# Optimization experiments

Hardware: AMD Instinct MI355X
Metric: run time of the kernel (lower is better)

## Reference

```python
import jax, jax.numpy as jnp
import numpy as np

T, B, I, H, O = 512, 64, 512, 1024, 512


def setup_inputs() -> dict:
    key = jax.random.key(0)
    ks = jax.random.split(key, 12)
    k = 1.0 / np.sqrt(H)  # torch LSTM/Linear init scale
    u = lambda kk, shape: jax.random.uniform(kk, shape, jnp.float32, -k, k)
    return {
        "x": jax.random.normal(ks[0], (T, B, I), jnp.float32),
        # layer 0 (input -> hidden)
        "W_ih0": u(ks[1], (4 * H, I)),
        "W_hh0": u(ks[2], (4 * H, H)),
        "b_ih0": u(ks[3], (4 * H,)),
        "b_hh0": u(ks[4], (4 * H,)),
        # layer 1 (hidden -> hidden)
        "W_ih1": u(ks[5], (4 * H, H)),
        "W_hh1": u(ks[6], (4 * H, H)),
        "b_ih1": u(ks[7], (4 * H,)),
        "b_hh1": u(ks[8], (4 * H,)),
        # output projection
        "W_out": u(ks[9], (O, H)),
        "b_out": u(ks[10], (O,)),
    }


def _lstm_layer(x_seq, W_ih, W_hh, b_ih, b_hh):
    """x_seq: [T, B, in]; returns hidden sequence [T, B, H].
    PyTorch gate order: i, f, g, o."""
    Hh = W_hh.shape[1]
    Bb = x_seq.shape[1]
    # precompute input contribution for all timesteps (one big GEMM)
    pre = jnp.einsum('tbi,gi->tbg', x_seq, W_ih) + b_ih + b_hh  # [T, B, 4H]

    def step(carry, pre_t):
        h, c = carry
        gates = pre_t + h @ W_hh.T  # [B, 4H]
        i, f, g, o = jnp.split(gates, 4, axis=-1)
        i = jax.nn.sigmoid(i)
        f = jax.nn.sigmoid(f)
        g = jnp.tanh(g)
        o = jax.nn.sigmoid(o)
        c = f * c + i * g
        h = o * jnp.tanh(c)
        return (h, c), h

    h0 = jnp.zeros((Bb, Hh), x_seq.dtype)
    c0 = jnp.zeros((Bb, Hh), x_seq.dtype)
    _, hs = jax.lax.scan(step, (h0, c0), pre)
    return hs  # [T, B, H]


def reference(x, W_ih0, W_hh0, b_ih0, b_hh0, W_ih1, W_hh1, b_ih1, b_hh1, W_out, b_out):
    h1 = _lstm_layer(x, W_ih0, W_hh0, b_ih0, b_hh0)   # [T, B, H]
    h2 = _lstm_layer(h1, W_ih1, W_hh1, b_ih1, b_hh1)  # [T, B, H]
    return jnp.einsum('tbh,oh->tbo', h2, W_out) + b_out  # [T, B, O]
```

## Files before the change

kernel.cpp:

```cpp
#include <hip/hip_runtime.h>
#include <hip/hip_bf16.h>
#include <cstdint>
#include <cstddef>

typedef short bf16x8 __attribute__((ext_vector_type(8)));
typedef float f32x4  __attribute__((ext_vector_type(4)));
typedef __hip_bfloat16 bf16;

#define NT_T 512
#define NB   64
#define NI   512
#define NH   1024
#define NO   512

static constexpr size_t SLOT_E = (size_t)NB * NH + 128;
static constexpr size_t SLOT_B = SLOT_E * 2;

static constexpr size_t OFF_XBF   = 0;
static constexpr size_t SZ_XBF    = (size_t)NT_T * NB * NI * 2;
static constexpr size_t OFF_WSW0  = OFF_XBF + SZ_XBF;
static constexpr size_t SZ_WSW0   = 128ull * 98304;
static constexpr size_t OFF_WSW1  = OFF_WSW0 + SZ_WSW0;
static constexpr size_t SZ_WSW1   = 128ull * 131072;
static constexpr size_t OFF_WOUT  = OFF_WSW1 + SZ_WSW1;
static constexpr size_t SZ_WOUT   = (size_t)NO * NH * 2;
static constexpr size_t OFF_B0    = OFF_WOUT + SZ_WOUT;
static constexpr size_t OFF_B1    = OFF_B0 + 4096 * 4;
static constexpr size_t OFF_H1    = OFF_B1 + 4096 * 4;
static constexpr size_t SZ_H1     = (size_t)NT_T * SLOT_B;
static constexpr size_t OFF_H2    = OFF_H1 + SZ_H1;
static constexpr size_t SZ_H2     = (size_t)NT_T * SLOT_B;
static constexpr size_t OFF_FLG   = OFF_H2 + SZ_H2;
static constexpr size_t SZ_FLG    = 2ull * 128 * 512 * 2;

__device__ __forceinline__ float sigm(float x) {
  return 1.0f / (1.0f + __expf(-x));
}
__device__ __forceinline__ float tanh_fast(float x) {
  x = fminf(15.0f, fmaxf(-15.0f, x));
  const float e = __expf(2.0f * x);
  return (e - 1.0f) / (e + 1.0f);
}

__device__ __forceinline__ void waitf1(const unsigned short* f) {
  while (!__all(__hip_atomic_load(f, __ATOMIC_RELAXED, __HIP_MEMORY_SCOPE_AGENT) != 0))
    __builtin_amdgcn_s_sleep(1);
  asm volatile("" ::: "memory");
}
__device__ __forceinline__ void waitf2(const unsigned short* f0, const unsigned short* f1) {
  while (true) {
    const int a = __hip_atomic_load(f0, __ATOMIC_RELAXED, __HIP_MEMORY_SCOPE_AGENT);
    const int b = __hip_atomic_load(f1, __ATOMIC_RELAXED, __HIP_MEMORY_SCOPE_AGENT);
    if (__all((a != 0) && (b != 0))) break;
    __builtin_amdgcn_s_sleep(1);
  }
  asm volatile("" ::: "memory");
}

template <int N>
__device__ __forceinline__ void load_batch(bf16x8 (&A)[N][2], const bf16* p0, const bf16* p1) {
#pragma unroll
  for (int i = 0; i < N; ++i) {
    A[i][0] = *(const bf16x8*)(p0 + i * 32);
    A[i][1] = *(const bf16x8*)(p1 + i * 32);
  }
}

template <int N, int KSW>
__device__ __forceinline__ void mfma_batch(f32x4 (&acc)[2][2], const bf16x8 (&A)[N][2],
                                           const char* Wlds, int ksbase, int lane) {
#pragma unroll
  for (int i = 0; i < N; ++i) {
#pragma unroll
    for (int nt = 0; nt < 2; ++nt) {
      const bf16x8 b = *(const bf16x8*)(Wlds + ((size_t)(nt * KSW + ksbase + i) * 64 + lane) * 16);
      acc[0][nt] = __builtin_amdgcn_mfma_f32_16x16x32_bf16(A[i][0], b, acc[0][nt], 0, 0, 0);
      acc[1][nt] = __builtin_amdgcn_mfma_f32_16x16x32_bf16(A[i][1], b, acc[1][nt], 0, 0, 0);
    }
  }
}

__global__ void k_convert_x(const float* __restrict__ x, bf16* __restrict__ xbf) {
  const size_t n = (size_t)NT_T * NB * NI;
  for (size_t i = (size_t)blockIdx.x * blockDim.x + threadIdx.x; i < n;
       i += (size_t)gridDim.x * blockDim.x)
    xbf[i] = __float2bfloat16(x[i]);
}

__global__ void k_build_wsw(const float* __restrict__ Wih0, const float* __restrict__ Whh0,
                            const float* __restrict__ Wih1, const float* __restrict__ Whh1,
                            bf16* __restrict__ wsw0, bf16* __restrict__ wsw1) {
  const size_t L0N = 128ull * 2 * 48 * 64 * 8;
  const size_t L1N = 128ull * 2 * 64 * 64 * 8;
  const size_t n = L0N + L1N;
  for (size_t i = (size_t)blockIdx.x * blockDim.x + threadIdx.x; i < n;
       i += (size_t)gridDim.x * blockDim.x) {
    if (i < L0N) {
      size_t idx = i;
      const int j = idx & 7;    idx >>= 3;
      const int lane = idx & 63; idx >>= 6;
      const int ks = (int)(idx % 48); idx /= 48;
      const int nt = idx & 1;
      const int blk = (int)(idx >> 1);
      const int nl = nt * 16 + (lane & 15);
      const int k = ks * 32 + (lane >> 4) * 8 + j;
      const int grow = (nl >> 3) * 1024 + blk * 8 + (nl & 7);
      const float v = (k < 512) ? Wih0[(size_t)grow * 512 + k]
                                : Whh0[(size_t)grow * 1024 + (k - 512)];
      wsw0[i] = __float2bfloat16(v);
    } else {
      size_t idx = i - L0N;
      const size_t o = idx;
      const int j = idx & 7;    idx >>= 3;
      const int lane = idx & 63; idx >>= 6;
      const int ks = (int)(idx % 64); idx /= 64;
      const int nt = idx & 1;
      const int blk = (int)(idx >> 1);
      const int nl = nt * 16 + (lane & 15);
      const int k = ks * 32 + (lane >> 4) * 8 + j;
      const int grow = (nl >> 3) * 1024 + blk * 8 + (nl & 7);
      const float v = (k < 1024) ? Wih1[(size_t)grow * 1024 + k]
                                 : Whh1[(size_t)grow * 1024 + (k - 1024)];
      wsw1[o] = __float2bfloat16(v);
    }
  }
}

__global__ void k_small(const float* __restrict__ Wout,
                        const float* __restrict__ bih0, const float* __restrict__ bhh0,
                        const float* __restrict__ bih1, const float* __restrict__ bhh1,
                        bf16* __restrict__ woutbf, float* __restrict__ bias0,
                        float* __restrict__ bias1, unsigned int* __restrict__ flg) {
  const int i = blockIdx.x * 256 + threadIdx.x;
  if (i < NO * NH) woutbf[i] = __float2bfloat16(Wout[i]);
  if (i < 4096) {
    bias0[i] = bih0[i] + bhh0[i];
    bias1[i] = bih1[i] + bhh1[i];
  }
  if (i < (int)(SZ_FLG / 4)) flg[i] = 0u;
}

__global__ __launch_bounds__(256, 1) void lstm_recur(
    const bf16* __restrict__ xbf, const bf16* __restrict__ wsw0, const bf16* __restrict__ wsw1,
    const float* __restrict__ bias0, const float* __restrict__ bias1,
    bf16* __restrict__ h1hist, bf16* __restrict__ h2hist, unsigned short* __restrict__ flg) {
  __shared__ char Wlds[131072];
  __shared__ float red[64][33];

  const int tid = threadIdx.x;
  const int bid = blockIdx.x;
  const int layer = bid >> 7;
  const int blk = bid & 127;
  const int lane = tid & 63;
  const int wid = tid >> 6;
  const int mh = wid & 1;
  const int kh = wid >> 1;
  const int q = lane >> 4;
  const int ml = lane & 15;
  const int colbase = blk * 8;
  const int row0 = mh * 32 + ml;
  const int row1 = mh * 32 + 16 + ml;

  {
    const char* src = layer ? (const char*)wsw1 + (size_t)blk * 131072
                            : (const char*)wsw0 + (size_t)blk * 98304;
    const int nb = layer ? 131072 : 98304;
    for (int off = tid * 16; off < nb; off += 256 * 16)
      *(uint4*)(Wlds + off) = *(const uint4*)(src + off);
  }

  float biasv[2];
  {
    const float* bs = layer ? bias1 : bias0;
#pragma unroll
    for (int nt = 0; nt < 2; ++nt) {
      const int nl = nt * 16 + ml;
      biasv[nt] = bs[(nl >> 3) * 1024 + colbase + (nl & 7)];
    }
  }
  __syncthreads();

  float cstate[2] = {0.f, 0.f};
  const f32x4 zacc = {0.f, 0.f, 0.f, 0.f};
  const char* WldsC = Wlds;

  const unsigned short* f_l0 = flg;
  const unsigned short* f_l1 = flg + ((size_t)128 << 9);
  unsigned short* fme = flg + (((size_t)layer * 128 + blk) << 9);

  for (int t = 0; t < NT_T; ++t) {
    const bf16* h1prev = h1hist + (size_t)(t - 1) * SLOT_E;
    const bf16* h1cur  = h1hist + (size_t)t * SLOT_E;
    const bf16* h2prev = h2hist + (size_t)(t - 1) * SLOT_E;

    f32x4 acc[2][2];
#pragma unroll
    for (int a1 = 0; a1 < 2; ++a1)
#pragma unroll
      for (int a2 = 0; a2 < 2; ++a2) acc[a1][a2] = zacc;

    if (layer == 0) {
      const bf16* xb = xbf + (size_t)t * NB * NI;
      const int kx = kh * 256 + q * 8;
      bf16x8 Ax[8][2];
      load_batch<8>(Ax, xb + (size_t)row0 * NI + kx, xb + (size_t)row1 * NI + kx);
      if (t > 0) {
        waitf1(f_l0 + (((size_t)(kh * 64 + lane)) << 9) + (t - 1));
        const int khh = kh * 512 + q * 8;
        bf16x8 Ah[16][2];
        load_batch<16>(Ah, h1prev + (size_t)row0 * NH + khh,
                       h1prev + (size_t)row1 * NH + khh);
        __builtin_amdgcn_sched_barrier(0);
        mfma_batch<8, 48>(acc, Ax, WldsC, kh * 8, lane);
        mfma_batch<16, 48>(acc, Ah, WldsC, 16 + kh * 16, lane);
      } else {
        __builtin_amdgcn_sched_barrier(0);
        mfma_batch<8, 48>(acc, Ax, WldsC, kh * 8, lane);
      }
    } else {
      if (kh == 0) {
        waitf2(f_l0 + ((size_t)lane << 9) + t,
               f_l0 + (((size_t)(64 + lane)) << 9) + t);
        bf16x8 Ah[32][2];
        load_batch<32>(Ah, h1cur + (size_t)row0 * NH + q * 8,
                       h1cur + (size_t)row1 * NH + q * 8);
        __builtin_amdgcn_sched_barrier(0);
        mfma_batch<32, 64>(acc, Ah, WldsC, 0, lane);
      } else if (t > 0) {
        waitf2(f_l1 + ((size_t)lane << 9) + (t - 1),
               f_l1 + (((size_t)(64 + lane)) << 9) + (t - 1));
        bf16x8 Ah[32][2];
        load_batch<32>(Ah, h2prev + (size_t)row0 * NH + q * 8,
                       h2prev + (size_t)row1 * NH + q * 8);
        __builtin_amdgcn_sched_barrier(0);
        mfma_batch<32, 64>(acc, Ah, WldsC, 32, lane);
      }
    }

    if (kh == 1) {
#pragma unroll
      for (int mt = 0; mt < 2; ++mt)
#pragma unroll
        for (int nt = 0; nt < 2; ++nt)
#pragma unroll
          for (int r = 0; r < 4; ++r)
            red[mh * 32 + mt * 16 + q * 4 + r][nt * 16 + ml] = acc[mt][nt][r];
    }
    __syncthreads();
    if (kh == 0) {
#pragma unroll
      for (int mt = 0; mt < 2; ++mt)
#pragma unroll
        for (int nt = 0; nt < 2; ++nt)
#pragma unroll
          for (int r = 0; r < 4; ++r) {
            const int mloc = mh * 32 + mt * 16 + q * 4 + r;
            const int nloc = nt * 16 + ml;
            red[mloc][nloc] = acc[mt][nt][r] + red[mloc][nloc] + biasv[nt];
          }
    }
    __syncthreads();

    {
      const int b = tid >> 2;
      const int cc0 = (tid & 3) * 2;
      unsigned short hb[2];
#pragma unroll
      for (int e2 = 0; e2 < 2; ++e2) {
        const int cc = cc0 + e2;
        const float gi = red[b][cc];
        const float gf = red[b][8 + cc];
        const float gg = red[b][16 + cc];
        const float go = red[b][24 + cc];
        const float cn = sigm(gf) * cstate[e2] + sigm(gi) * tanh_fast(gg);
        cstate[e2] = cn;
        const float hv = sigm(go) * tanh_fast(cn);
        hb[e2] = __builtin_bit_cast(unsigned short, __float2bfloat16(hv));
      }
      const unsigned int packed = (unsigned int)hb[0] | ((unsigned int)hb[1] << 16);
      bf16* dstbase = (layer ? h2hist : h1hist) + (size_t)t * SLOT_E + (size_t)b * NH;
      __hip_atomic_store((unsigned int*)(dstbase + colbase + cc0), packed,
                         __ATOMIC_RELAXED, __HIP_MEMORY_SCOPE_AGENT);
    }

    __syncthreads();
    if (tid == 0)
      __hip_atomic_store(fme + t, (unsigned short)1,
                         __ATOMIC_RELAXED, __HIP_MEMORY_SCOPE_AGENT);
  }
}

__global__ __launch_bounds__(256) void gemm_out(
    const bf16* __restrict__ A, const bf16* __restrict__ B,
    const float* __restrict__ bout, float* __restrict__ out) {
  __shared__ char As[8192];
  __shared__ char Bs[8192];
  const int tid = threadIdx.x;
  const int lane = tid & 63;
  const int wid = tid >> 6;
  const int wm = wid >> 1;
  const int wn = wid & 1;
  const size_t Mbase = (size_t)blockIdx.y * 128;
  const int Nbase = blockIdx.x * 128;

  const f32x4 zacc = {0.f, 0.f, 0.f, 0.f};
  f32x4 acc[4][4];
#pragma unroll
  for (int i = 0; i < 4; ++i)
#pragma unroll
    for (int j = 0; j < 4; ++j) acc[i][j] = zacc;

  for (int kc = 0; kc < 32; ++kc) {
    const int kb = kc * 32;
#pragma unroll
    for (int e = 0; e < 2; ++e) {
      const int id = e * 256 + tid;
      const int r = id >> 2;
      const int c8 = (id & 3) * 8;
      const int dst = ((r >> 4) * 64 + (c8 >> 3) * 16 + (r & 15)) * 16;
      const size_t m = Mbase + r;
      const bf16* arow = A + (m >> 6) * SLOT_E + (size_t)(m & 63) * NH;
      *(uint4*)(As + dst) = *(const uint4*)(arow + kb + c8);
      *(uint4*)(Bs + dst) = *(const uint4*)(B + (size_t)(Nbase + r) * NH + kb + c8);
    }
    __syncthreads();
    bf16x8 af[4], bfr[4];
#pragma unroll
    for (int i = 0; i < 4; ++i) {
      af[i]  = *(const bf16x8*)(As + ((wm * 4 + i) * 64 + lane) * 16);
      bfr[i] = *(const bf16x8*)(Bs + ((wn * 4 + i) * 64 + lane) * 16);
    }
#pragma unroll
    for (int i = 0; i < 4; ++i)
#pragma unroll
      for (int j = 0; j < 4; ++j)
        acc[i][j] = __builtin_amdgcn_mfma_f32_16x16x32_bf16(af[i], bfr[j], acc[i][j], 0, 0, 0);
    __syncthreads();
  }
  const int qq = lane >> 4, ml = lane & 15;
#pragma unroll
  for (int i = 0; i < 4; ++i)
#pragma unroll
    for (int j = 0; j < 4; ++j)
#pragma unroll
      for (int r = 0; r < 4; ++r) {
        const size_t m = Mbase + wm * 64 + i * 16 + qq * 4 + r;
        const int n = Nbase + wn * 64 + j * 16 + ml;
        out[m * NO + n] = acc[i][j][r] + bout[n];
      }
}

extern "C" void kernel_launch(void* const* d_in, const int* in_sizes, int n_in,
                              void* d_out, int out_size, void* d_ws, size_t ws_size,
                              hipStream_t stream) {
  (void)in_sizes; (void)n_in; (void)out_size; (void)ws_size;
  const float* x    = (const float*)d_in[0];
  const float* Wih0 = (const float*)d_in[1];
  const float* Whh0 = (const float*)d_in[2];
  const float* bih0 = (const float*)d_in[3];
  const float* bhh0 = (const float*)d_in[4];
  const float* Wih1 = (const float*)d_in[5];
  const float* Whh1 = (const float*)d_in[6];
  const float* bih1 = (const float*)d_in[7];
  const float* bhh1 = (const float*)d_in[8];
  const float* Wout = (const float*)d_in[9];
  const float* bout = (const float*)d_in[10];
  float* out = (float*)d_out;
  char* ws = (char*)d_ws;

  bf16*  xbf    = (bf16*)(ws + OFF_XBF);
  bf16*  wsw0   = (bf16*)(ws + OFF_WSW0);
  bf16*  wsw1   = (bf16*)(ws + OFF_WSW1);
  bf16*  woutbf = (bf16*)(ws + OFF_WOUT);
  float* bias0  = (float*)(ws + OFF_B0);
  float* bias1  = (float*)(ws + OFF_B1);
  bf16*  h1hist = (bf16*)(ws + OFF_H1);
  bf16*  h2hist = (bf16*)(ws + OFF_H2);
  unsigned short* flg = (unsigned short*)(ws + OFF_FLG);

  k_convert_x<<<8192, 256, 0, stream>>>(x, xbf);
  k_build_wsw<<<14336, 256, 0, stream>>>(Wih0, Whh0, Wih1, Whh1, wsw0, wsw1);
  k_small<<<2048, 256, 0, stream>>>(Wout, bih0, bhh0, bih1, bhh1, woutbf, bias0, bias1,
                                    (unsigned int*)flg);
  lstm_recur<<<256, 256, 0, stream>>>(xbf, wsw0, wsw1, bias0, bias1, h1hist, h2hist, flg);
  gemm_out<<<dim3(4, 256), 256, 0, stream>>>(h2hist, woutbf, bout, out);
}
```

Before: 5.488 ms.

## Replace per-step flag handshake with sentinel-filled hidden state polling

Removes the separate flag array and the per-block flag store after each timestep. The hidden-state history buffers are pre-filled with an all-ones sentinel, and consumers poll the actual h data with atomic loads until no 32-bit word equals the sentinel. This folds the dependency wait and the data load into one step, cutting a round trip through flag memory on the serial recurrence path. The cost is a fill kernel over both history buffers and heavier polling traffic. It relies on a packed bf16 pair never being 0xFFFFFFFF, which would be a NaN pair.

```diff
diff --git a/kernel.cpp b/kernel.cpp
--- a/kernel.cpp
+++ b/kernel.cpp
@@ -5,6 +5,7 @@
 
 typedef short bf16x8 __attribute__((ext_vector_type(8)));
 typedef float f32x4  __attribute__((ext_vector_type(4)));
+typedef unsigned int u32x4 __attribute__((ext_vector_type(4)));
 typedef __hip_bfloat16 bf16;
 
 #define NT_T 512
@@ -30,8 +31,6 @@
 static constexpr size_t SZ_H1     = (size_t)NT_T * SLOT_B;
 static constexpr size_t OFF_H2    = OFF_H1 + SZ_H1;
 static constexpr size_t SZ_H2     = (size_t)NT_T * SLOT_B;
-static constexpr size_t OFF_FLG   = OFF_H2 + SZ_H2;
-static constexpr size_t SZ_FLG    = 2ull * 128 * 512 * 2;
 
 __device__ __forceinline__ float sigm(float x) {
   return 1.0f / (1.0f + __expf(-x));
@@ -42,18 +41,37 @@
   return (e - 1.0f) / (e + 1.0f);
 }
 
-__device__ __forceinline__ void waitf1(const unsigned short* f) {
-  while (!__all(__hip_atomic_load(f, __ATOMIC_RELAXED, __HIP_MEMORY_SCOPE_AGENT) != 0))
+template <int N>
+__device__ __forceinline__ void poll_tile(bf16x8 (&A)[N][2], const bf16* p0, const bf16* p1) {
+  const unsigned int* q0 = (const unsigned int*)p0;
+  const unsigned int* q1 = (const unsigned int*)p1;
+  unsigned int V[N][2][4];
+  while (true) {
+#pragma unroll
+    for (int i = 0; i < N; ++i)
+#pragma unroll
+      for (int j = 0; j < 4; ++j) {
+        V[i][0][j] = __hip_atomic_load(q0 + i * 16 + j, __ATOMIC_RELAXED, __HIP_MEMORY_SCOPE_AGENT);
+        V[i][1][j] = __hip_atomic_load(q1 + i * 16 + j, __ATOMIC_RELAXED, __HIP_MEMORY_SCOPE_AGENT);
+      }
+    bool ok = true;
+#pragma unroll
+    for (int i = 0; i < N; ++i)
+#pragma unroll
+      for (int r = 0; r < 2; ++r)
+#pragma unroll
+        for (int j = 0; j < 4; ++j)
+          ok &= (V[i][r][j] != 0xFFFFFFFFu);
+    if (__all(ok)) break;
     __builtin_amdgcn_s_sleep(1);
-  asm volatile("" ::: "memory");
-}
-__device__ __forceinline__ void waitf2(const unsigned short* f0, const unsigned short* f1) {
-  while (true) {
-    const int a = __hip_atomic_load(f0, __ATOMIC_RELAXED, __HIP_MEMORY_SCOPE_AGENT);
-    const int b = __hip_atomic_load(f1, __ATOMIC_RELAXED, __HIP_MEMORY_SCOPE_AGENT);
-    if (__all((a != 0) && (b != 0))) break;
-    __builtin_amdgcn_s_sleep(1);
-  }
+  }
+#pragma unroll
+  for (int i = 0; i < N; ++i)
+#pragma unroll
+    for (int r = 0; r < 2; ++r) {
+      const u32x4 tv = {V[i][r][0], V[i][r][1], V[i][r][2], V[i][r][3]};
+      A[i][r] = __builtin_bit_cast(bf16x8, tv);
+    }
   asm volatile("" ::: "memory");
 }
 
@@ -85,6 +103,13 @@
   for (size_t i = (size_t)blockIdx.x * blockDim.x + threadIdx.x; i < n;
        i += (size_t)gridDim.x * blockDim.x)
     xbf[i] = __float2bfloat16(x[i]);
+}
+
+__global__ void k_fill(u32x4* __restrict__ p, size_t n16) {
+  const u32x4 s = {0xFFFFFFFFu, 0xFFFFFFFFu, 0xFFFFFFFFu, 0xFFFFFFFFu};
+  for (size_t i = (size_t)blockIdx.x * blockDim.x + threadIdx.x; i < n16;
+       i += (size_t)gridDim.x * blockDim.x)
+    p[i] = s;
 }
 
 __global__ void k_build_wsw(const float* __restrict__ Wih0, const float* __restrict__ Whh0,
@@ -130,20 +155,19 @@
                         const float* __restrict__ bih0, const float* __restrict__ bhh0,
                         const float* __restrict__ bih1, const float* __restrict__ bhh1,
                         bf16* __restrict__ woutbf, float* __restrict__ bias0,
-                        float* __restrict__ bias1, unsigned int* __restrict__ flg) {
+                        float* __restrict__ bias1) {
   const int i = blockIdx.x * 256 + threadIdx.x;
   if (i < NO * NH) woutbf[i] = __float2bfloat16(Wout[i]);
   if (i < 4096) {
     bias0[i] = bih0[i] + bhh0[i];
     bias1[i] = bih1[i] + bhh1[i];
   }
-  if (i < (int)(SZ_FLG / 4)) flg[i] = 0u;
 }
 
 __global__ __launch_bounds__(256, 1) void lstm_recur(
     const bf16* __restrict__ xbf, const bf16* __restrict__ wsw0, const bf16* __restrict__ wsw1,
     const float* __restrict__ bias0, const float* __restrict__ bias1,
-    bf16* __restrict__ h1hist, bf16* __restrict__ h2hist, unsigned short* __restrict__ flg) {
+    bf16* __restrict__ h1hist, bf16* __restrict__ h2hist) {
   __shared__ char Wlds[131072];
   __shared__ float red[64][33];
 
@@ -184,10 +208,6 @@
   const f32x4 zacc = {0.f, 0.f, 0.f, 0.f};
   const char* WldsC = Wlds;
 
-  const unsigned short* f_l0 = flg;
-  const unsigned short* f_l1 = flg + ((size_t)128 << 9);
-  unsigned short* fme = flg + (((size_t)layer * 128 + blk) << 9);
-
   for (int t = 0; t < NT_T; ++t) {
     const bf16* h1prev = h1hist + (size_t)(t - 1) * SLOT_E;
     const bf16* h1cur  = h1hist + (size_t)t * SLOT_E;
@@ -205,35 +225,33 @@
       bf16x8 Ax[8][2];
       load_batch<8>(Ax, xb + (size_t)row0 * NI + kx, xb + (size_t)row1 * NI + kx);
       if (t > 0) {
-        waitf1(f_l0 + (((size_t)(kh * 64 + lane)) << 9) + (t - 1));
-        const int khh = kh * 512 + q * 8;
         bf16x8 Ah[16][2];
-        load_batch<16>(Ah, h1prev + (size_t)row0 * NH + khh,
-                       h1prev + (size_t)row1 * NH + khh);
-        __builtin_amdgcn_sched_barrier(0);
+        poll_tile<16>(Ah, h1prev + (size_t)row0 * NH + kh * 512 + q * 8,
+                          h1prev + (size_t)row1 * NH + kh * 512 + q * 8);
         mfma_batch<8, 48>(acc, Ax, WldsC, kh * 8, lane);
         mfma_batch<16, 48>(acc, Ah, WldsC, 16 + kh * 16, lane);
       } else {
-        __builtin_amdgcn_sched_barrier(0);
         mfma_batch<8, 48>(acc, Ax, WldsC, kh * 8, lane);
       }
     } else {
       if (kh == 0) {
-        waitf2(f_l0 + ((size_t)lane << 9) + t,
-               f_l0 + (((size_t)(64 + lane)) << 9) + t);
-        bf16x8 Ah[32][2];
-        load_batch<32>(Ah, h1cur + (size_t)row0 * NH + q * 8,
-                       h1cur + (size_t)row1 * NH + q * 8);
-        __builtin_amdgcn_sched_barrier(0);
-        mfma_batch<32, 64>(acc, Ah, WldsC, 0, lane);
+        bf16x8 A0[16][2];
+        poll_tile<16>(A0, h1cur + (size_t)row0 * NH + q * 8,
+                          h1cur + (size_t)row1 * NH + q * 8);
+        mfma_batch<16, 64>(acc, A0, WldsC, 0, lane);
+        bf16x8 A1[16][2];
+        poll_tile<16>(A1, h1cur + (size_t)row0 * NH + 512 + q * 8,
+                          h1cur + (size_t)row1 * NH + 512 + q * 8);
+        mfma_batch<16, 64>(acc, A1, WldsC, 16, lane);
       } else if (t > 0) {
-        waitf2(f_l1 + ((size_t)lane << 9) + (t - 1),
-               f_l1 + (((size_t)(64 + lane)) << 9) + (t - 1));
-        bf16x8 Ah[32][2];
-        load_batch<32>(Ah, h2prev + (size_t)row0 * NH + q * 8,
-                       h2prev + (size_t)row1 * NH + q * 8);
-        __builtin_amdgcn_sched_barrier(0);
-        mfma_batch<32, 64>(acc, Ah, WldsC, 32, lane);
+        bf16x8 A0[16][2];
+        poll_tile<16>(A0, h2prev + (size_t)row0 * NH + q * 8,
+                          h2prev + (size_t)row1 * NH + q * 8);
+        mfma_batch<16, 64>(acc, A0, WldsC, 32, lane);
+        bf16x8 A1[16][2];
+        poll_tile<16>(A1, h2prev + (size_t)row0 * NH + 512 + q * 8,
+                          h2prev + (size_t)row1 * NH + 512 + q * 8);
+        mfma_batch<16, 64>(acc, A1, WldsC, 48, lane);
       }
     }
 
@@ -284,9 +302,6 @@
     }
 
     __syncthreads();
-    if (tid == 0)
-      __hip_atomic_store(fme + t, (unsigned short)1,
-                         __ATOMIC_RELAXED, __HIP_MEMORY_SCOPE_AGENT);
   }
 }
 
@@ -376,12 +391,11 @@
   float* bias1  = (float*)(ws + OFF_B1);
   bf16*  h1hist = (bf16*)(ws + OFF_H1);
   bf16*  h2hist = (bf16*)(ws + OFF_H2);
-  unsigned short* flg = (unsigned short*)(ws + OFF_FLG);
 
   k_convert_x<<<8192, 256, 0, stream>>>(x, xbf);
+  k_fill<<<8192, 256, 0, stream>>>((u32x4*)(ws + OFF_H1), (SZ_H1 + SZ_H2) / 16);
   k_build_wsw<<<14336, 256, 0, stream>>>(Wih0, Whh0, Wih1, Whh1, wsw0, wsw1);
-  k_small<<<2048, 256, 0, stream>>>(Wout, bih0, bhh0, bih1, bhh1, woutbf, bias0, bias1,
-                                    (unsigned int*)flg);
-  lstm_recur<<<256, 256, 0, stream>>>(xbf, wsw0, wsw1, bias0, bias1, h1hist, h2hist, flg);
+  k_small<<<2048, 256, 0, stream>>>(Wout, bih0, bhh0, bih1, bhh1, woutbf, bias0, bias1);
+  lstm_recur<<<256, 256, 0, stream>>>(xbf, wsw0, wsw1, bias0, bias1, h1hist, h2hist);
   gemm_out<<<dim3(4, 256), 256, 0, stream>>>(h2hist, woutbf, bout, out);
 }
```

Measured after the change: 17.80 ms. 224% more time.

## Split LSTM recurrence into per-batch-group wave pairs with fine-grained flags

Applied to the files above, without the earlier changes.

Each workgroup doubles to 512 threads, organised as four 16-row batch groups of two waves each. Within a group the two waves split K, and partial sums meet through LDS guarded by a workgroup-scope flag instead of block-wide __syncthreads. Completion flags are kept per group, so consumer waves in other blocks wait only on the 16 batch rows they read, not on the whole block. This lets batch groups run out of lockstep across the step-to-step dependency chain. The cost is four times as many global flags to poll and more spinning on LDS flags, and there is some risk of a memory-ordering race on the double-buffered partial sums.

```diff
diff --git a/kernel.cpp b/kernel.cpp
--- a/kernel.cpp
+++ b/kernel.cpp
@@ -31,7 +31,7 @@
 static constexpr size_t OFF_H2    = OFF_H1 + SZ_H1;
 static constexpr size_t SZ_H2     = (size_t)NT_T * SLOT_B;
 static constexpr size_t OFF_FLG   = OFF_H2 + SZ_H2;
-static constexpr size_t SZ_FLG    = 2ull * 128 * 512 * 2;
+static constexpr size_t SZ_FLG    = 2ull * 128 * 4 * 512 * 2;
 
 __device__ __forceinline__ float sigm(float x) {
   return 1.0f / (1.0f + __expf(-x));
@@ -42,11 +42,6 @@
   return (e - 1.0f) / (e + 1.0f);
 }
 
-__device__ __forceinline__ void waitf1(const unsigned short* f) {
-  while (!__all(__hip_atomic_load(f, __ATOMIC_RELAXED, __HIP_MEMORY_SCOPE_AGENT) != 0))
-    __builtin_amdgcn_s_sleep(1);
-  asm volatile("" ::: "memory");
-}
 __device__ __forceinline__ void waitf2(const unsigned short* f0, const unsigned short* f1) {
   while (true) {
     const int a = __hip_atomic_load(f0, __ATOMIC_RELAXED, __HIP_MEMORY_SCOPE_AGENT);
@@ -58,24 +53,20 @@
 }
 
 template <int N>
-__device__ __forceinline__ void load_batch(bf16x8 (&A)[N][2], const bf16* p0, const bf16* p1) {
-#pragma unroll
-  for (int i = 0; i < N; ++i) {
-    A[i][0] = *(const bf16x8*)(p0 + i * 32);
-    A[i][1] = *(const bf16x8*)(p1 + i * 32);
-  }
+__device__ __forceinline__ void load_frags(bf16x8 (&A)[N], const bf16* p) {
+#pragma unroll
+  for (int i = 0; i < N; ++i) A[i] = *(const bf16x8*)(p + i * 32);
 }
 
 template <int N, int KSW>
-__device__ __forceinline__ void mfma_batch(f32x4 (&acc)[2][2], const bf16x8 (&A)[N][2],
+__device__ __forceinline__ void mfma_frags(f32x4 (&acc)[2], const bf16x8 (&A)[N],
                                            const char* Wlds, int ksbase, int lane) {
 #pragma unroll
   for (int i = 0; i < N; ++i) {
 #pragma unroll
     for (int nt = 0; nt < 2; ++nt) {
       const bf16x8 b = *(const bf16x8*)(Wlds + ((size_t)(nt * KSW + ksbase + i) * 64 + lane) * 16);
-      acc[0][nt] = __builtin_amdgcn_mfma_f32_16x16x32_bf16(A[i][0], b, acc[0][nt], 0, 0, 0);
-      acc[1][nt] = __builtin_amdgcn_mfma_f32_16x16x32_bf16(A[i][1], b, acc[1][nt], 0, 0, 0);
+      acc[nt] = __builtin_amdgcn_mfma_f32_16x16x32_bf16(A[i], b, acc[nt], 0, 0, 0);
     }
   }
 }
@@ -140,12 +131,14 @@
   if (i < (int)(SZ_FLG / 4)) flg[i] = 0u;
 }
 
-__global__ __launch_bounds__(256, 1) void lstm_recur(
+__global__ __launch_bounds__(512, 1) void lstm_recur(
     const bf16* __restrict__ xbf, const bf16* __restrict__ wsw0, const bf16* __restrict__ wsw1,
     const float* __restrict__ bias0, const float* __restrict__ bias1,
     bf16* __restrict__ h1hist, bf16* __restrict__ h2hist, unsigned short* __restrict__ flg) {
   __shared__ char Wlds[131072];
-  __shared__ float red[64][33];
+  __shared__ float grpP[2][4][2][16][16];
+  __shared__ float grpG[4][16][33];
+  __shared__ int grpFlag[4][16];
 
   const int tid = threadIdx.x;
   const int bid = blockIdx.x;
@@ -153,19 +146,18 @@
   const int blk = bid & 127;
   const int lane = tid & 63;
   const int wid = tid >> 6;
-  const int mh = wid & 1;
-  const int kh = wid >> 1;
+  const int g = wid >> 1;
+  const int kh = wid & 1;
   const int q = lane >> 4;
   const int ml = lane & 15;
   const int colbase = blk * 8;
-  const int row0 = mh * 32 + ml;
-  const int row1 = mh * 32 + 16 + ml;
+  const int rb = g * 16;
 
   {
     const char* src = layer ? (const char*)wsw1 + (size_t)blk * 131072
                             : (const char*)wsw0 + (size_t)blk * 98304;
     const int nb = layer ? 131072 : 98304;
-    for (int off = tid * 16; off < nb; off += 256 * 16)
+    for (int off = tid * 16; off < nb; off += 512 * 16)
       *(uint4*)(Wlds + off) = *(const uint4*)(src + off);
   }
 
@@ -178,115 +170,108 @@
       biasv[nt] = bs[(nl >> 3) * 1024 + colbase + (nl & 7)];
     }
   }
+  if (tid < 64) ((int*)grpFlag)[tid] = 0;
   __syncthreads();
 
+  const int KS = layer ? 64 : 48;
   float cstate[2] = {0.f, 0.f};
   const f32x4 zacc = {0.f, 0.f, 0.f, 0.f};
   const char* WldsC = Wlds;
 
   const unsigned short* f_l0 = flg;
-  const unsigned short* f_l1 = flg + ((size_t)128 << 9);
-  unsigned short* fme = flg + (((size_t)layer * 128 + blk) << 9);
+  const unsigned short* f_l1 = flg + (size_t)128 * 4 * 512;
+  unsigned short* fme = flg + ((((size_t)layer * 128 + blk) * 4 + g) << 9);
 
   for (int t = 0; t < NT_T; ++t) {
     const bf16* h1prev = h1hist + (size_t)(t - 1) * SLOT_E;
     const bf16* h1cur  = h1hist + (size_t)t * SLOT_E;
     const bf16* h2prev = h2hist + (size_t)(t - 1) * SLOT_E;
 
-    f32x4 acc[2][2];
-#pragma unroll
-    for (int a1 = 0; a1 < 2; ++a1)
-#pragma unroll
-      for (int a2 = 0; a2 < 2; ++a2) acc[a1][a2] = zacc;
+    f32x4 acc[2];
+    acc[0] = zacc; acc[1] = zacc;
 
     if (layer == 0) {
-      const bf16* xb = xbf + (size_t)t * NB * NI;
-      const int kx = kh * 256 + q * 8;
-      bf16x8 Ax[8][2];
-      load_batch<8>(Ax, xb + (size_t)row0 * NI + kx, xb + (size_t)row1 * NI + kx);
-      if (t > 0) {
-        waitf1(f_l0 + (((size_t)(kh * 64 + lane)) << 9) + (t - 1));
-        const int khh = kh * 512 + q * 8;
-        bf16x8 Ah[16][2];
-        load_batch<16>(Ah, h1prev + (size_t)row0 * NH + khh,
-                       h1prev + (size_t)row1 * NH + khh);
+      if (kh == 0) {
+        const bf16* xb = xbf + (size_t)t * NB * NI + (size_t)(rb + ml) * NI + q * 8;
+        bf16x8 Ax[16];
+        load_frags<16>(Ax, xb);
         __builtin_amdgcn_sched_barrier(0);
-        mfma_batch<8, 48>(acc, Ax, WldsC, kh * 8, lane);
-        mfma_batch<16, 48>(acc, Ah, WldsC, 16 + kh * 16, lane);
-      } else {
+        mfma_frags<16, 48>(acc, Ax, WldsC, 0, lane);
+      } else if (t > 0) {
+        waitf2(f_l0 + (((size_t)lane * 4 + g) << 9) + (t - 1),
+               f_l0 + (((size_t)(64 + lane) * 4 + g) << 9) + (t - 1));
+        const bf16* hb = h1prev + (size_t)(rb + ml) * NH + q * 8;
+        bf16x8 Ah[32];
+        load_frags<32>(Ah, hb);
         __builtin_amdgcn_sched_barrier(0);
-        mfma_batch<8, 48>(acc, Ax, WldsC, kh * 8, lane);
+        mfma_frags<32, 48>(acc, Ah, WldsC, 16, lane);
       }
     } else {
       if (kh == 0) {
-        waitf2(f_l0 + ((size_t)lane << 9) + t,
-               f_l0 + (((size_t)(64 + lane)) << 9) + t);
-        bf16x8 Ah[32][2];
-        load_batch<32>(Ah, h1cur + (size_t)row0 * NH + q * 8,
-                       h1cur + (size_t)row1 * NH + q * 8);
+        waitf2(f_l0 + (((size_t)lane * 4 + g) << 9) + t,
+               f_l0 + (((size_t)(64 + lane) * 4 + g) << 9) + t);
+        const bf16* hb = h1cur + (size_t)(rb + ml) * NH + q * 8;
+        bf16x8 Ah[32];
+        load_frags<32>(Ah, hb);
         __builtin_amdgcn_sched_barrier(0);
-        mfma_batch<32, 64>(acc, Ah, WldsC, 0, lane);
+        mfma_frags<32, 64>(acc, Ah, WldsC, 0, lane);
       } else if (t > 0) {
-        waitf2(f_l1 + ((size_t)lane << 9) + (t - 1),
-               f_l1 + (((size_t)(64 + lane)) << 9) + (t - 1));
-        bf16x8 Ah[32][2];
-        load_batch<32>(Ah, h2prev + (size_t)row0 * NH + q * 8,
-                       h2prev + (size_t)row1 * NH + q * 8);
+        waitf2(f_l1 + (((size_t)lane * 4 + g) << 9) + (t - 1),
+               f_l1 + (((size_t)(64 + lane) * 4 + g) << 9) + (t - 1));
+        const bf16* hb = h2prev + (size_t)(rb + ml) * NH + q * 8;
+        bf16x8 Ah[32];
+        load_frags<32>(Ah, hb);
         __builtin_amdgcn_sched_barrier(0);
-        mfma_batch<32, 64>(acc, Ah, WldsC, 32, lane);
+        mfma_frags<32, 64>(acc, Ah, WldsC, 32, lane);
       }
     }
 
     if (kh == 1) {
 #pragma unroll
-      for (int mt = 0; mt < 2; ++mt)
-#pragma unroll
-        for (int nt = 0; nt < 2; ++nt)
-#pragma unroll
-          for (int r = 0; r < 4; ++r)
-            red[mh * 32 + mt * 16 + q * 4 + r][nt * 16 + ml] = acc[mt][nt][r];
-    }
-    __syncthreads();
-    if (kh == 0) {
-#pragma unroll
-      for (int mt = 0; mt < 2; ++mt)
-#pragma unroll
-        for (int nt = 0; nt < 2; ++nt)
-#pragma unroll
-          for (int r = 0; r < 4; ++r) {
-            const int mloc = mh * 32 + mt * 16 + q * 4 + r;
-            const int nloc = nt * 16 + ml;
-            red[mloc][nloc] = acc[mt][nt][r] + red[mloc][nloc] + biasv[nt];
-          }
-    }
-    __syncthreads();
-
-    {
-      const int b = tid >> 2;
-      const int cc0 = (tid & 3) * 2;
-      unsigned short hb[2];
+      for (int nt = 0; nt < 2; ++nt)
+#pragma unroll
+        for (int r = 0; r < 4; ++r)
+          grpP[t & 1][g][nt][q * 4 + r][ml] = acc[nt][r];
+      asm volatile("s_waitcnt lgkmcnt(0)" ::: "memory");
+      __hip_atomic_store(&grpFlag[g][0], t + 1, __ATOMIC_RELAXED, __HIP_MEMORY_SCOPE_WORKGROUP);
+    } else {
+      while (__hip_atomic_load(&grpFlag[g][0], __ATOMIC_RELAXED,
+                               __HIP_MEMORY_SCOPE_WORKGROUP) < t + 1) {}
+      asm volatile("" ::: "memory");
+#pragma unroll
+      for (int nt = 0; nt < 2; ++nt)
+#pragma unroll
+        for (int r = 0; r < 4; ++r)
+          grpG[g][q * 4 + r][nt * 16 + ml] =
+              acc[nt][r] + grpP[t & 1][g][nt][q * 4 + r][ml] + biasv[nt];
+      asm volatile("s_waitcnt lgkmcnt(0)" ::: "memory");
+
+      const int b16 = lane >> 2;
+      const int cc0 = (lane & 3) * 2;
+      unsigned short hb2[2];
 #pragma unroll
       for (int e2 = 0; e2 < 2; ++e2) {
         const int cc = cc0 + e2;
-        const float gi = red[b][cc];
-        const float gf = red[b][8 + cc];
-        const float gg = red[b][16 + cc];
-        const float go = red[b][24 + cc];
+        const float gi = grpG[g][b16][cc];
+        const float gf = grpG[g][b16][8 + cc];
+        const float gg = grpG[g][b16][16 + cc];
+        const float go = grpG[g][b16][24 + cc];
         const float cn = sigm(gf) * cstate[e2] + sigm(gi) * tanh_fast(gg);
         cstate[e2] = cn;
         const float hv = sigm(go) * tanh_fast(cn);
-        hb[e2] = __builtin_bit_cast(unsigned short, __float2bfloat16(hv));
+        hb2[e2] = __builtin_bit_cast(unsigned short, __float2bfloat16(hv));
       }
-      const unsigned int packed = (unsigned int)hb[0] | ((unsigned int)hb[1] << 16);
-      bf16* dstbase = (layer ? h2hist : h1hist) + (size_t)t * SLOT_E + (size_t)b * NH;
+      const unsigned int packed = (unsigned int)hb2[0] | ((unsigned int)hb2[1] << 16);
+      bf16* dstbase = (layer ? h2hist : h1hist) + (size_t)t * SLOT_E
+                      + (size_t)(rb + b16) * NH;
       __hip_atomic_store((unsigned int*)(dstbase + colbase + cc0), packed,
                          __ATOMIC_RELAXED, __HIP_MEMORY_SCOPE_AGENT);
-    }
-
-    __syncthreads();
-    if (tid == 0)
-      __hip_atomic_store(fme + t, (unsigned short)1,
-                         __ATOMIC_RELAXED, __HIP_MEMORY_SCOPE_AGENT);
+
+      asm volatile("s_waitcnt vmcnt(0)" ::: "memory");
+      if (lane == 0)
+        __hip_atomic_store(fme + t, (unsigned short)1,
+                           __ATOMIC_RELAXED, __HIP_MEMORY_SCOPE_AGENT);
+    }
   }
 }
 
@@ -382,6 +367,6 @@
   k_build_wsw<<<14336, 256, 0, stream>>>(Wih0, Whh0, Wih1, Whh1, wsw0, wsw1);
   k_small<<<2048, 256, 0, stream>>>(Wout, bih0, bhh0, bih1, bhh1, woutbf, bias0, bias1,
                                     (unsigned int*)flg);
-  lstm_recur<<<256, 256, 0, stream>>>(xbf, wsw0, wsw1, bias0, bias1, h1hist, h2hist, flg);
+  lstm_recur<<<256, 512, 0, stream>>>(xbf, wsw0, wsw1, bias0, bias1, h1hist, h2hist, flg);
   gemm_out<<<dim3(4, 256), 256, 0, stream>>>(h2hist, woutbf, bout, out);
 }
```

New measurement: 6.191 ms. +12.8%, slower.

## Validate hidden-state loads against a sentinel fill and signal step flags before barrier

Applied to the files above, without the earlier changes.

Fills the h1/h2 history buffers with an all-ones sentinel pattern, then checks each loaded hidden-state tile for it. Any lane that sees the sentinel re-polls that location with atomic loads until real data arrives. The per-step completion flag is now stored before the trailing __syncthreads rather than after it, and the sched_barrier calls are removed. The aim is to publish step readiness earlier so consumers can proceed sooner and rely on the sentinel check for correctness. The costs are an extra fill pass over the history buffers, per-load comparison work, a compare in gemm_out's A loads, and a window where the flag can precede other warps' h stores.

```diff
diff --git a/kernel.cpp b/kernel.cpp
--- a/kernel.cpp
+++ b/kernel.cpp
@@ -5,6 +5,7 @@
 
 typedef short bf16x8 __attribute__((ext_vector_type(8)));
 typedef float f32x4  __attribute__((ext_vector_type(4)));
+typedef unsigned int u32x4 __attribute__((ext_vector_type(4)));
 typedef __hip_bfloat16 bf16;
 
 #define NT_T 512
@@ -66,6 +67,41 @@
   }
 }
 
+template <int N>
+__device__ __forceinline__ void validate_tile(bf16x8 (&A)[N][2],
+                                              const bf16* p0, const bf16* p1) {
+  unsigned agg = 0;
+#pragma unroll
+  for (int i = 0; i < N; ++i)
+#pragma unroll
+    for (int r = 0; r < 2; ++r) {
+      const u32x4 d = __builtin_bit_cast(u32x4, A[i][r]);
+      agg |= (unsigned)(d[0] == 0xFFFFFFFFu) | (unsigned)(d[1] == 0xFFFFFFFFu) |
+             (unsigned)(d[2] == 0xFFFFFFFFu) | (unsigned)(d[3] == 0xFFFFFFFFu);
+    }
+  if (!__any(agg != 0)) return;
+  for (int i = 0; i < N; ++i)
+    for (int r = 0; r < 2; ++r) {
+      const unsigned* q = (const unsigned*)((r ? p1 : p0) + i * 32);
+      while (true) {
+        const u32x4 d = __builtin_bit_cast(u32x4, A[i][r]);
+        const bool bad = (d[0] == 0xFFFFFFFFu) | (d[1] == 0xFFFFFFFFu) |
+                         (d[2] == 0xFFFFFFFFu) | (d[3] == 0xFFFFFFFFu);
+        if (!__any(bad)) break;
+        if (bad) {
+          u32x4 nd;
+          nd[0] = __hip_atomic_load(q + 0, __ATOMIC_RELAXED, __HIP_MEMORY_SCOPE_AGENT);
+          nd[1] = __hip_atomic_load(q + 1, __ATOMIC_RELAXED, __HIP_MEMORY_SCOPE_AGENT);
+          nd[2] = __hip_atomic_load(q + 2, __ATOMIC_RELAXED, __HIP_MEMORY_SCOPE_AGENT);
+          nd[3] = __hip_atomic_load(q + 3, __ATOMIC_RELAXED, __HIP_MEMORY_SCOPE_AGENT);
+          A[i][r] = __builtin_bit_cast(bf16x8, nd);
+        }
+        __builtin_amdgcn_s_sleep(1);
+      }
+    }
+  asm volatile("" ::: "memory");
+}
+
 template <int N, int KSW>
 __device__ __forceinline__ void mfma_batch(f32x4 (&acc)[2][2], const bf16x8 (&A)[N][2],
                                            const char* Wlds, int ksbase, int lane) {
@@ -85,6 +121,13 @@
   for (size_t i = (size_t)blockIdx.x * blockDim.x + threadIdx.x; i < n;
        i += (size_t)gridDim.x * blockDim.x)
     xbf[i] = __float2bfloat16(x[i]);
+}
+
+__global__ void k_fill(u32x4* __restrict__ p, size_t n16) {
+  const u32x4 s = {0xFFFFFFFFu, 0xFFFFFFFFu, 0xFFFFFFFFu, 0xFFFFFFFFu};
+  for (size_t i = (size_t)blockIdx.x * blockDim.x + threadIdx.x; i < n16;
+       i += (size_t)gridDim.x * blockDim.x)
+    p[i] = s;
 }
 
 __global__ void k_build_wsw(const float* __restrict__ Wih0, const float* __restrict__ Whh0,
@@ -207,32 +250,34 @@
       if (t > 0) {
         waitf1(f_l0 + (((size_t)(kh * 64 + lane)) << 9) + (t - 1));
         const int khh = kh * 512 + q * 8;
+        const bf16* hp0 = h1prev + (size_t)row0 * NH + khh;
+        const bf16* hp1 = h1prev + (size_t)row1 * NH + khh;
         bf16x8 Ah[16][2];
-        load_batch<16>(Ah, h1prev + (size_t)row0 * NH + khh,
-                       h1prev + (size_t)row1 * NH + khh);
-        __builtin_amdgcn_sched_barrier(0);
+        load_batch<16>(Ah, hp0, hp1);
+        validate_tile<16>(Ah, hp0, hp1);
         mfma_batch<8, 48>(acc, Ax, WldsC, kh * 8, lane);
         mfma_batch<16, 48>(acc, Ah, WldsC, 16 + kh * 16, lane);
       } else {
-        __builtin_amdgcn_sched_barrier(0);
         mfma_batch<8, 48>(acc, Ax, WldsC, kh * 8, lane);
       }
     } else {
       if (kh == 0) {
         waitf2(f_l0 + ((size_t)lane << 9) + t,
                f_l0 + (((size_t)(64 + lane)) << 9) + t);
+        const bf16* hp0 = h1cur + (size_t)row0 * NH + q * 8;
+        const bf16* hp1 = h1cur + (size_t)row1 * NH + q * 8;
         bf16x8 Ah[32][2];
-        load_batch<32>(Ah, h1cur + (size_t)row0 * NH + q * 8,
-                       h1cur + (size_t)row1 * NH + q * 8);
-        __builtin_amdgcn_sched_barrier(0);
+        load_batch<32>(Ah, hp0, hp1);
+        validate_tile<32>(Ah, hp0, hp1);
         mfma_batch<32, 64>(acc, Ah, WldsC, 0, lane);
       } else if (t > 0) {
         waitf2(f_l1 + ((size_t)lane << 9) + (t - 1),
                f_l1 + (((size_t)(64 + lane)) << 9) + (t - 1));
+        const bf16* hp0 = h2prev + (size_t)row0 * NH + q * 8;
+        const bf16* hp1 = h2prev + (size_t)row1 * NH + q * 8;
         bf16x8 Ah[32][2];
-        load_batch<32>(Ah, h2prev + (size_t)row0 * NH + q * 8,
-                       h2prev + (size_t)row1 * NH + q * 8);
-        __builtin_amdgcn_sched_barrier(0);
+        load_batch<32>(Ah, hp0, hp1);
+        validate_tile<32>(Ah, hp0, hp1);
         mfma_batch<32, 64>(acc, Ah, WldsC, 32, lane);
       }
     }
@@ -283,10 +328,11 @@
                          __ATOMIC_RELAXED, __HIP_MEMORY_SCOPE_AGENT);
     }
 
-    __syncthreads();
     if (tid == 0)
       __hip_atomic_store(fme + t, (unsigned short)1,
                          __ATOMIC_RELAXED, __HIP_MEMORY_SCOPE_AGENT);
+
+    __syncthreads();
   }
 }
 
@@ -320,7 +366,21 @@
       const int dst = ((r >> 4) * 64 + (c8 >> 3) * 16 + (r & 15)) * 16;
       const size_t m = Mbase + r;
       const bf16* arow = A + (m >> 6) * SLOT_E + (size_t)(m & 63) * NH;
-      *(uint4*)(As + dst) = *(const uint4*)(arow + kb + c8);
+      uint4 va = *(const uint4*)(arow + kb + c8);
+      {
+        const unsigned bad = (unsigned)(va.x == 0xFFFFFFFFu) | (unsigned)(va.y == 0xFFFFFFFFu) |
+                             (unsigned)(va.z == 0xFFFFFFFFu) | (unsigned)(va.w == 0xFFFFFFFFu);
+        if (__any(bad != 0)) {
+          const unsigned* q = (const unsigned*)(arow + kb + c8);
+          if (bad) {
+            va.x = __hip_atomic_load(q + 0, __ATOMIC_RELAXED, __HIP_MEMORY_SCOPE_AGENT);
+            va.y = __hip_atomic_load(q + 1, __ATOMIC_RELAXED, __HIP_MEMORY_SCOPE_AGENT);
+            va.z = __hip_atomic_load(q + 2, __ATOMIC_RELAXED, __HIP_MEMORY_SCOPE_AGENT);
+            va.w = __hip_atomic_load(q + 3, __ATOMIC_RELAXED, __HIP_MEMORY_SCOPE_AGENT);
+          }
+        }
+      }
+      *(uint4*)(As + dst) = va;
       *(uint4*)(Bs + dst) = *(const uint4*)(B + (size_t)(Nbase + r) * NH + kb + c8);
     }
     __syncthreads();
@@ -379,6 +439,7 @@
   unsigned short* flg = (unsigned short*)(ws + OFF_FLG);
 
   k_convert_x<<<8192, 256, 0, stream>>>(x, xbf);
+  k_fill<<<8192, 256, 0, stream>>>((u32x4*)(ws + OFF_H1), (SZ_H1 + SZ_H2) / 16);
   k_build_wsw<<<14336, 256, 0, stream>>>(Wih0, Whh0, Wih1, Whh1, wsw0, wsw1);
   k_small<<<2048, 256, 0, stream>>>(Wout, bih0, bhh0, bih1, bhh1, woutbf, bias0, bias1,
                                     (unsigned int*)flg);
```

Result: slower. 16.69 ms (+204.2%).
